# Kernel tuning notes

Measured on AMD Instinct MI355X. Metric: run time of the kernel, lower is better.

## Reference

```python
import jax, jax.numpy as jnp
import numpy as np

B, T, D = 2, 2048, 1024
H, HD = 16, 64
DL, DC = 512, 256
THETA = 10000.0
LN_EPS = 1e-5


def setup_inputs() -> dict:
    key = jax.random.key(0)
    ks = jax.random.split(key, 8)
    s = 0.02
    return {
        "x": jax.random.normal(ks[0], (B, T, D), jnp.float32),
        "W_q": jax.random.normal(ks[1], (H * HD, D), jnp.float32) * s,
        "b_q": jnp.zeros((H * HD,), jnp.float32),
        "W_kvl": jax.random.normal(ks[2], (DL, D), jnp.float32) * s,
        "b_kvl": jnp.zeros((DL,), jnp.float32),
        "ts_scale": jnp.ones((DL,), jnp.float32),
        "ts_shift": jnp.zeros((DL,), jnp.float32),
        "W_comp": jax.random.normal(ks[3], (DC, DL), jnp.float32) * s,
        "W_exp": jax.random.normal(ks[4], (DL, DC), jnp.float32) * s,
        "ln_g": jnp.ones((DC,), jnp.float32),
        "ln_b": jnp.zeros((DC,), jnp.float32),
        "W_fkv": jax.random.normal(ks[5], (2 * H * HD, DL), jnp.float32) * s,
        "b_fkv": jnp.zeros((2 * H * HD,), jnp.float32),
        "W_out": jax.random.normal(ks[6], (D, H * HD), jnp.float32) * s,
        "b_out": jnp.zeros((D,), jnp.float32),
    }


def _rope_tables(t_len):
    inv_freq = 1.0 / (THETA ** (jnp.arange(0, HD, 2, dtype=jnp.float32) / HD))
    pos = jnp.arange(t_len, dtype=jnp.float32)
    freqs = pos[:, None] * inv_freq[None, :]          # [T, HD/2]
    cos = jnp.concatenate([jnp.cos(freqs)] * 2, -1)   # [T, HD]
    sin = jnp.concatenate([jnp.sin(freqs)] * 2, -1)
    return cos[None, None], sin[None, None]           # [1,1,T,HD]


def _rotate_half(z):
    return jnp.concatenate([-z[..., HD // 2:], z[..., :HD // 2]], -1)


def reference(x, W_q, b_q, W_kvl, b_kvl, ts_scale, ts_shift, W_comp, W_exp,
              ln_g, ln_b, W_fkv, b_fkv, W_out, b_out):
    # Q path: [B,T,D] -> [B,H,T,HD]
    q = (jnp.einsum('btd,ed->bte', x, W_q) + b_q).reshape(B, T, H, HD).transpose(0, 2, 1, 3)

    # KV latent + learned KVSplice bottleneck
    kvl = jnp.einsum('btd,ld->btl', x, W_kvl) + b_kvl                 # [B,T,DL]
    xt = kvl * jax.nn.softplus(ts_scale) + ts_shift
    c = jnp.einsum('btl,cl->btc', xt, W_comp)                         # [B,T,DC]
    mu = jnp.mean(c, -1, keepdims=True)
    var = jnp.mean(jnp.square(c - mu), -1, keepdims=True)
    c = (c - mu) * jax.lax.rsqrt(var + LN_EPS) * ln_g + ln_b
    dec = jnp.einsum('btc,lc->btl', c, W_exp)                         # [B,T,DL]

    # Decompress latent to K,V
    kv = jnp.einsum('btl,el->bte', dec, W_fkv) + b_fkv                # [B,T,2*H*HD]
    kv = kv.reshape(B, T, 2, H, HD).transpose(2, 0, 3, 1, 4)          # [2,B,H,T,HD]
    k, v = kv[0], kv[1]

    # RoPE
    cos, sin = _rope_tables(T)
    q = q * cos + _rotate_half(q) * sin
    k = k * cos + _rotate_half(k) * sin

    # Causal SDPA
    scale = 1.0 / np.sqrt(HD)
    scores = jnp.einsum('bhqd,bhkd->bhqk', q, k) * scale
    mask = jnp.tril(jnp.ones((T, T), bool))
    scores = jnp.where(mask, scores, jnp.float32(-1e30))
    attn = jax.nn.softmax(scores, axis=-1)
    o = jnp.einsum('bhqk,bhkd->bhqd', attn, v)
    o = o.transpose(0, 2, 1, 3).reshape(B, T, H * HD)
    return jnp.einsum('bte,de->btd', o, W_out) + b_out
```

## Files before the change

### kernel.cpp

```cpp
#include <hip/hip_runtime.h>
#include <math.h>

#define B_SZ   2
#define T_SEQ  2048
#define NH     16
#define HDIM   64
#define D_MOD  1024
#define DL     512
#define DC     256
#define MROWS  4096

typedef __attribute__((ext_vector_type(8))) short bf16x8;
typedef __attribute__((ext_vector_type(4))) float f32x4;

#define SCALE_Q 0.18033688011112042f

static __device__ __forceinline__ unsigned short f2bf(float f) {
    union { float f; unsigned u; } v; v.f = f;
    unsigned r = v.u + 0x7fffu + ((v.u >> 16) & 1u);
    return (unsigned short)(r >> 16);
}

static __device__ __forceinline__ void gl_lds16(const unsigned short* g,
                                                unsigned short* l) {
    __builtin_amdgcn_global_load_lds(
        (const __attribute__((address_space(1))) unsigned int*)g,
        (__attribute__((address_space(3))) unsigned int*)l, 16, 0, 0);
}

__global__ __launch_bounds__(256) void cvt_bf16(
    const float* __restrict__ x,  const float* __restrict__ wq,
    const float* __restrict__ wkvl, const float* __restrict__ wcomp,
    const float* __restrict__ wexp, const float* __restrict__ wfkv,
    const float* __restrict__ wout,
    unsigned short* __restrict__ xb,  unsigned short* __restrict__ wqh,
    unsigned short* __restrict__ wkvlh, unsigned short* __restrict__ wcomph,
    unsigned short* __restrict__ wexph, unsigned short* __restrict__ wfkvh,
    unsigned short* __restrict__ wouth, float2* __restrict__ rope_tab)
{
    const int g = blockIdx.x * 256 + threadIdx.x;
    const int stride = gridDim.x * 256;
#define CVT_SEG(src, dst, n4)                                              \
    for (int i = g; i < (n4); i += stride) {                               \
        float4 v = ((const float4*)(src))[i];                              \
        unsigned short h[4] = {f2bf(v.x), f2bf(v.y), f2bf(v.z), f2bf(v.w)};\
        *(uint2*)((dst) + (size_t)i * 4) = *(uint2*)h;                     \
    }
    CVT_SEG(x, xb, 1048576)
    CVT_SEG(wq, wqh, 262144)
    CVT_SEG(wkvl, wkvlh, 131072)
    CVT_SEG(wcomp, wcomph, 32768)
    CVT_SEG(wexp, wexph, 32768)
    CVT_SEG(wfkv, wfkvh, 262144)
    CVT_SEG(wout, wouth, 262144)
#undef CVT_SEG
    for (int i = g; i < T_SEQ * 32; i += stride) {
        const int t = i >> 5, fi = i & 31;
        const float inv = __expf((float)fi * (-9.210340371976184f / 32.0f));
        float sn, cs; sincosf((float)t * inv, &sn, &cs);
        rope_tab[i] = make_float2(cs, sn);
    }
}

#define GEMM64R_PROLOG(Aptr, Wptr, Kdim)                                       \
    __shared__ unsigned short As[64 * 64];                                     \
    __shared__ unsigned short Ws[64 * 64];                                     \
    const int tid = threadIdx.x;                                               \
    const int w = tid >> 6, lane = tid & 63;                                   \
    const int l16 = lane & 15, quad = lane >> 4;                               \
    const int sw8 = ((lane & 7) ^ ((lane >> 3) & 7)) << 3;                     \
    const int srow = lane >> 3;                                                \
    const unsigned short* Ag0 = (Aptr) + (size_t)(m0 + w * 16 + srow) * (Kdim) + sw8;      \
    const unsigned short* Ag1 = (Aptr) + (size_t)(m0 + w * 16 + 8 + srow) * (Kdim) + sw8;  \
    const unsigned short* Wg0 = (Wptr) + (size_t)(n0 + w * 16 + srow) * (Kdim) + sw8;      \
    const unsigned short* Wg1 = (Wptr) + (size_t)(n0 + w * 16 + 8 + srow) * (Kdim) + sw8;  \
    unsigned short* Al0 = &As[(w * 16) * 64];                                  \
    unsigned short* Al1 = &As[(w * 16 + 8) * 64];                              \
    unsigned short* Wl0 = &Ws[(w * 16) * 64];                                  \
    unsigned short* Wl1 = &Ws[(w * 16 + 8) * 64];                              \
    const int xh = (l16 & 7);                                                  \
    f32x4 acc[4];                                                              \
    _Pragma("unroll") for (int j = 0; j < 4; ++j)                              \
        acc[j] = (f32x4){0.f, 0.f, 0.f, 0.f};                                  \
    for (int k0 = 0; k0 < (Kdim); k0 += 64) {                                  \
        __syncthreads();                                                       \
        gl_lds16(Ag0 + k0, Al0);                                               \
        gl_lds16(Ag1 + k0, Al1);                                               \
        gl_lds16(Wg0 + k0, Wl0);                                               \
        gl_lds16(Wg1 + k0, Wl1);                                               \
        __syncthreads();                                                       \
        bf16x8 af[2], bfr[4][2];                                               \
        _Pragma("unroll") for (int kk = 0; kk < 2; ++kk)                       \
            af[kk] = *(const bf16x8*)&As[(w * 16 + l16) * 64 +                 \
                                         (((kk * 4 + quad) ^ xh) << 3)];       \
        _Pragma("unroll") for (int j = 0; j < 4; ++j)                          \
            _Pragma("unroll") for (int kk = 0; kk < 2; ++kk)                   \
                bfr[j][kk] = *(const bf16x8*)&Ws[(j * 16 + l16) * 64 +         \
                                             (((kk * 4 + quad) ^ xh) << 3)];   \
        _Pragma("unroll") for (int kk = 0; kk < 2; ++kk)                       \
            _Pragma("unroll") for (int j = 0; j < 4; ++j)                      \
                acc[j] = __builtin_amdgcn_mfma_f32_16x16x32_bf16(              \
                    af[kk], bfr[j][kk], acc[j], 0, 0, 0);                      \
    }

__global__ __launch_bounds__(256) void gemm_qxt(
    const unsigned short* __restrict__ A, const unsigned short* __restrict__ Wq,
    const unsigned short* __restrict__ Wkvl,
    const float* __restrict__ b_q, const float* __restrict__ b_kvl,
    const float* __restrict__ ts_scale, const float* __restrict__ ts_shift,
    const float2* __restrict__ tab,
    unsigned short* __restrict__ qh, unsigned short* __restrict__ xt)
{
    const int m0 = blockIdx.x * 64;
    const bool is_q = (blockIdx.y < 16);
    const int n0 = is_q ? blockIdx.y * 64 : (blockIdx.y - 16) * 64;
    const unsigned short* W = is_q ? Wq : Wkvl;

    GEMM64R_PROLOG(A, W, D_MOD)

    if (is_q) {
#pragma unroll
        for (int j = 0; j < 4; ++j) {
            const int col = n0 + j * 16 + l16;
            const int h = col >> 6, hd = col & 63;
            const float bv = b_q[col];
            const float bvp = b_q[col ^ 32];
            const float sgn = (hd < 32) ? -1.f : 1.f;
#pragma unroll
            for (int reg = 0; reg < 4; ++reg) {
                const int row = m0 + w * 16 + quad * 4 + reg;
                const int b = row >> 11, t = row & (T_SEQ - 1);
                const float2 cssn = tab[t * 32 + (hd & 31)];
                const float v  = acc[j][reg] + bv;
                const float vp = acc[j ^ 2][reg] + bvp;
                const float r = (v * cssn.x + sgn * vp * cssn.y) * SCALE_Q;
                qh[(((size_t)b * NH + h) * T_SEQ + t) * HDIM + hd] = f2bf(r);
            }
        }
    } else {
#pragma unroll
        for (int j = 0; j < 4; ++j) {
            const int col = n0 + j * 16 + l16;
            const float bv = b_kvl[col];
            const float sp_s = log1pf(expf(ts_scale[col]));
            const float sp_t = ts_shift[col];
#pragma unroll
            for (int reg = 0; reg < 4; ++reg) {
                const int row = m0 + w * 16 + quad * 4 + reg;
                const float val = (acc[j][reg] + bv) * sp_s + sp_t;
                xt[(size_t)row * DL + col] = f2bf(val);
            }
        }
    }
}

__global__ __launch_bounds__(256) void gemm_kv(
    const unsigned short* __restrict__ A, const unsigned short* __restrict__ W,
    const float* __restrict__ bias, const float2* __restrict__ tab,
    unsigned short* __restrict__ kh, unsigned short* __restrict__ vth)
{
    const int m0 = blockIdx.x * 64, n0 = blockIdx.y * 64;

    GEMM64R_PROLOG(A, W, DL)

    if (n0 < 1024) {
#pragma unroll
        for (int j = 0; j < 4; ++j) {
            const int col = n0 + j * 16 + l16;
            const int h = (col >> 6) & 15, hd = col & 63;
            const float bv = bias[col];
            const float bvp = bias[col ^ 32];
            const float sgn = (hd < 32) ? -1.f : 1.f;
#pragma unroll
            for (int reg = 0; reg < 4; ++reg) {
                const int row = m0 + w * 16 + quad * 4 + reg;
                const int b = row >> 11, t = row & (T_SEQ - 1);
                const float2 cssn = tab[t * 32 + (hd & 31)];
                const float v  = acc[j][reg] + bv;
                const float vp = acc[j ^ 2][reg] + bvp;
                const float r = v * cssn.x + sgn * vp * cssn.y;
                kh[(((size_t)b * NH + h) * T_SEQ + t) * HDIM + hd] = f2bf(r);
            }
        }
    } else {
#pragma unroll
        for (int j = 0; j < 4; ++j) {
            const int col = n0 + j * 16 + l16;
            const int cv = col - 1024;
            const int h = cv >> 6, hd = cv & 63;
            const float bv = bias[col];
            unsigned short hv[4];
            const int r0 = m0 + w * 16 + quad * 4;
            const int b = r0 >> 11, t0 = r0 & (T_SEQ - 1);
#pragma unroll
            for (int reg = 0; reg < 4; ++reg)
                hv[reg] = f2bf(acc[j][reg] + bv);
            *(uint2*)&vth[(((size_t)b * NH + h) * HDIM + hd) * T_SEQ + t0] =
                *(uint2*)hv;
        }
    }
}

__global__ __launch_bounds__(256) void gemm_out(
    const unsigned short* __restrict__ A, const unsigned short* __restrict__ W,
    const float* __restrict__ bias, float* __restrict__ C)
{
    const int m0 = blockIdx.x * 64, n0 = blockIdx.y * 64;

    GEMM64R_PROLOG(A, W, D_MOD)

#pragma unroll
    for (int j = 0; j < 4; ++j) {
        const int col = n0 + j * 16 + l16;
        const float bv = bias[col];
#pragma unroll
        for (int reg = 0; reg < 4; ++reg) {
            const int row = m0 + w * 16 + quad * 4 + reg;
            C[(size_t)row * D_MOD + col] = acc[j][reg] + bv;
        }
    }
}

__global__ __launch_bounds__(256) void gemm_b(
    const unsigned short* __restrict__ A, const unsigned short* __restrict__ W,
    unsigned short* __restrict__ dec)
{
    const int m0 = blockIdx.x * 64, n0 = blockIdx.y * 64;

    GEMM64R_PROLOG(A, W, DC)

#pragma unroll
    for (int j = 0; j < 4; ++j) {
        const int col = n0 + j * 16 + l16;
#pragma unroll
        for (int reg = 0; reg < 4; ++reg) {
            const int row = m0 + w * 16 + quad * 4 + reg;
            dec[(size_t)row * DL + col] = f2bf(acc[j][reg]);
        }
    }
}

__global__ __launch_bounds__(256) void gemm_c_ln(
    const unsigned short* __restrict__ A, const unsigned short* __restrict__ W,
    const float* __restrict__ g, const float* __restrict__ bta,
    unsigned short* __restrict__ outb)
{
    __shared__ unsigned short As[16 * 32];
    __shared__ unsigned short Ws[256 * 32];
    __shared__ float redS[4][16];
    __shared__ float redQ[4][16];

    const int tid = threadIdx.x;
    const int w = tid >> 6, lane = tid & 63;
    const int l16 = lane & 15, quad = lane >> 4;
    const int m0 = blockIdx.x * 16;

    const int srow = lane >> 2, scol = (lane & 3) << 3;
    const unsigned short* Ag = A + (size_t)(m0 + srow) * DL + scol;
    const unsigned short* Wg = W + (size_t)(w * 64 + srow) * DL + scol;

    f32x4 acc[4];
#pragma unroll
    for (int j = 0; j < 4; ++j) acc[j] = (f32x4){0.f, 0.f, 0.f, 0.f};

    for (int k0 = 0; k0 < DL; k0 += 32) {
        __syncthreads();
        if (w == 0) gl_lds16(Ag + k0, &As[0]);
#pragma unroll
        for (int c = 0; c < 4; ++c)
            gl_lds16(Wg + (size_t)(c * 16) * DL + k0, &Ws[(w * 64 + c * 16) * 32]);
        __syncthreads();

        const bf16x8 af = *(const bf16x8*)&As[l16 * 32 + quad * 8];
        bf16x8 bfr[4];
#pragma unroll
        for (int j = 0; j < 4; ++j)
            bfr[j] = *(const bf16x8*)&Ws[(w * 64 + j * 16 + l16) * 32 + quad * 8];
#pragma unroll
        for (int j = 0; j < 4; ++j)
            acc[j] = __builtin_amdgcn_mfma_f32_16x16x32_bf16(af, bfr[j], acc[j], 0, 0, 0);
    }

    float s[4], q2[4];
#pragma unroll
    for (int reg = 0; reg < 4; ++reg) {
        float sv = (acc[0][reg] + acc[1][reg]) + (acc[2][reg] + acc[3][reg]);
        float qv = (acc[0][reg] * acc[0][reg] + acc[1][reg] * acc[1][reg]) +
                   (acc[2][reg] * acc[2][reg] + acc[3][reg] * acc[3][reg]);
#pragma unroll
        for (int off = 1; off < 16; off <<= 1) {
            sv += __shfl_xor(sv, off);
            qv += __shfl_xor(qv, off);
        }
        s[reg] = sv; q2[reg] = qv;
    }
    if (l16 == 0) {
#pragma unroll
        for (int reg = 0; reg < 4; ++reg) {
            redS[w][quad * 4 + reg] = s[reg];
            redQ[w][quad * 4 + reg] = q2[reg];
        }
    }
    __syncthreads();

#pragma unroll
    for (int reg = 0; reg < 4; ++reg) {
        const int r = quad * 4 + reg;
        const float sum = (redS[0][r] + redS[1][r]) + (redS[2][r] + redS[3][r]);
        const float sq  = (redQ[0][r] + redQ[1][r]) + (redQ[2][r] + redQ[3][r]);
        const float mu  = sum * (1.0f / DC);
        const float var = sq * (1.0f / DC) - mu * mu;
        const float rstd = rsqrtf(var + 1e-5f);
#pragma unroll
        for (int j = 0; j < 4; ++j) {
            const int col = w * 64 + j * 16 + l16;
            const float val = (acc[j][reg] - mu) * rstd * g[col] + bta[col];
            outb[(size_t)(m0 + r) * DC + col] = f2bf(val);
        }
    }
}

__global__ __launch_bounds__(256, 3) void flash_mfma(
    const unsigned short* __restrict__ q, const unsigned short* __restrict__ k,
    const unsigned short* __restrict__ vt, unsigned short* __restrict__ o)
{
    __shared__ unsigned short Ks[2][64 * 72];
    __shared__ unsigned short Vs[2][64 * 72];
    __shared__ unsigned short Ps[64 * 72];

    const int bh = blockIdx.x & 31;
    const int j  = 31 - (blockIdx.x >> 5);
    const int q0 = j * 64;
    const int tid = threadIdx.x;
    const int w = tid >> 6, lane = tid & 63;
    const int l16 = lane & 15, quad = lane >> 4;
    const int rbase = q0 + w * 16;

    bf16x8 qf[2];
#pragma unroll
    for (int kk = 0; kk < 2; ++kk)
        qf[kk] = *(const bf16x8*)(q + ((size_t)bh * T_SEQ + rbase + l16) * HDIM + kk * 32 + quad * 8);

    f32x4 of[4];
    float lrow[4];
#pragma unroll
    for (int dt = 0; dt < 4; ++dt) of[dt] = (f32x4){0.f, 0.f, 0.f, 0.f};
#pragma unroll
    for (int r = 0; r < 4; ++r) lrow[r] = 0.f;

    const int ldr = tid >> 2;
    const int ldc = (tid & 3) * 16;
    const unsigned short* kgb = k + ((size_t)bh * T_SEQ + ldr) * HDIM + ldc;
    const unsigned short* vgb = vt + ((size_t)bh * HDIM + ldr) * T_SEQ + ldc;

    bf16x8 kr0 = *(const bf16x8*)kgb;
    bf16x8 kr1 = *(const bf16x8*)(kgb + 8);
    bf16x8 vr0 = *(const bf16x8*)vgb;
    bf16x8 vr1 = *(const bf16x8*)(vgb + 8);

    const int kend = (j + 1) * 64;
    int buf = 0;
    for (int k0 = 0; k0 < kend; k0 += 64, buf ^= 1) {
        *(bf16x8*)&Ks[buf][ldr * 72 + ldc]     = kr0;
        *(bf16x8*)&Ks[buf][ldr * 72 + ldc + 8] = kr1;
        *(bf16x8*)&Vs[buf][ldr * 72 + ldc]     = vr0;
        *(bf16x8*)&Vs[buf][ldr * 72 + ldc + 8] = vr1;
        if (k0 + 64 < kend) {
            const unsigned short* kg = kgb + (size_t)(k0 + 64) * HDIM;
            const unsigned short* vg = vgb + (k0 + 64);
            kr0 = *(const bf16x8*)kg;
            kr1 = *(const bf16x8*)(kg + 8);
            vr0 = *(const bf16x8*)vg;
            vr1 = *(const bf16x8*)(vg + 8);
        }
        __syncthreads();

        bf16x8 kf[4][2];
#pragma unroll
        for (int nt = 0; nt < 4; ++nt)
#pragma unroll
            for (int kk = 0; kk < 2; ++kk)
                kf[nt][kk] = *(const bf16x8*)&Ks[buf][(nt * 16 + l16) * 72 + kk * 32 + quad * 8];

        f32x4 sf[4];
        __builtin_amdgcn_s_setprio(1);
#pragma unroll
        for (int nt = 0; nt < 4; ++nt) {
            sf[nt] = (f32x4){0.f, 0.f, 0.f, 0.f};
#pragma unroll
            for (int kk = 0; kk < 2; ++kk)
                sf[nt] = __builtin_amdgcn_mfma_f32_16x16x32_bf16(qf[kk], kf[nt][kk], sf[nt], 0, 0, 0);
        }
        __builtin_amdgcn_s_setprio(0);

        const bool need_mask = (k0 + 63) > rbase;
#pragma unroll
        for (int reg = 0; reg < 4; ++reg) {
            float a0 = sf[0][reg], a1 = sf[1][reg], a2 = sf[2][reg], a3 = sf[3][reg];
            if (need_mask) {
                const int tq = rbase + quad * 4 + reg;
                if (k0 +      l16 > tq) a0 = -1e30f;
                if (k0 + 16 + l16 > tq) a1 = -1e30f;
                if (k0 + 32 + l16 > tq) a2 = -1e30f;
                if (k0 + 48 + l16 > tq) a3 = -1e30f;
            }
            union { float f; unsigned u; } u0, u1, u2, u3;
            u0.f = exp2f(a0); u1.f = exp2f(a1);
            u2.f = exp2f(a2); u3.f = exp2f(a3);
            const int prow = (w * 16 + quad * 4 + reg) * 72 + l16;
            Ps[prow]      = (unsigned short)(u0.u >> 16);
            Ps[prow + 16] = (unsigned short)(u1.u >> 16);
            Ps[prow + 32] = (unsigned short)(u2.u >> 16);
            Ps[prow + 48] = (unsigned short)(u3.u >> 16);
            u0.u &= 0xffff0000u; u1.u &= 0xffff0000u;
            u2.u &= 0xffff0000u; u3.u &= 0xffff0000u;
            lrow[reg] += (u0.f + u1.f) + (u2.f + u3.f);
        }

        bf16x8 vf[4][2];
#pragma unroll
        for (int dt = 0; dt < 4; ++dt)
#pragma unroll
            for (int kk = 0; kk < 2; ++kk)
                vf[dt][kk] = *(const bf16x8*)&Vs[buf][(dt * 16 + l16) * 72 + kk * 32 + quad * 8];

        bf16x8 pf[2];
#pragma unroll
        for (int kk = 0; kk < 2; ++kk)
            pf[kk] = *(const bf16x8*)&Ps[(w * 16 + l16) * 72 + kk * 32 + quad * 8];
        __builtin_amdgcn_s_setprio(1);
#pragma unroll
        for (int dt = 0; dt < 4; ++dt)
#pragma unroll
            for (int kk = 0; kk < 2; ++kk)
                of[dt] = __builtin_amdgcn_mfma_f32_16x16x32_bf16(pf[kk], vf[dt][kk], of[dt], 0, 0, 0);
        __builtin_amdgcn_s_setprio(0);
    }

    const int b = bh >> 4, h = bh & 15;
#pragma unroll
    for (int reg = 0; reg < 4; ++reg) {
        float l = lrow[reg];
        l += __shfl_xor(l, 1);
        l += __shfl_xor(l, 2);
        l += __shfl_xor(l, 4);
        l += __shfl_xor(l, 8);
        const float inv = 1.0f / l;
        const int t = rbase + quad * 4 + reg;
#pragma unroll
        for (int dt = 0; dt < 4; ++dt)
            o[((size_t)b * T_SEQ + t) * (NH * HDIM) + h * HDIM + dt * 16 + l16] =
                f2bf(of[dt][reg] * inv);
    }
}

extern "C" void kernel_launch(void* const* d_in, const int* in_sizes, int n_in,
                              void* d_out, int out_size, void* d_ws, size_t ws_size,
                              hipStream_t stream)
{
    (void)in_sizes; (void)n_in; (void)out_size; (void)ws_size;

    const float* x        = (const float*)d_in[0];
    const float* W_q      = (const float*)d_in[1];
    const float* b_q      = (const float*)d_in[2];
    const float* W_kvl    = (const float*)d_in[3];
    const float* b_kvl    = (const float*)d_in[4];
    const float* ts_scale = (const float*)d_in[5];
    const float* ts_shift = (const float*)d_in[6];
    const float* W_comp   = (const float*)d_in[7];
    const float* W_exp    = (const float*)d_in[8];
    const float* ln_g     = (const float*)d_in[9];
    const float* ln_b     = (const float*)d_in[10];
    const float* W_fkv    = (const float*)d_in[11];
    const float* b_fkv    = (const float*)d_in[12];
    const float* W_out    = (const float*)d_in[13];
    const float* b_out    = (const float*)d_in[14];
    float* out = (float*)d_out;

    char* p = (char*)d_ws;
    unsigned short* xb     = (unsigned short*)p;             p += 8  * 1024 * 1024;
    unsigned short* wqh    = (unsigned short*)p;             p += 2  * 1024 * 1024;
    unsigned short* wkvlh  = (unsigned short*)p;             p += 1  * 1024 * 1024;
    unsigned short* wcomph = (unsigned short*)p;             p += 256 * 1024;
    unsigned short* wexph  = (unsigned short*)p;             p += 256 * 1024;
    unsigned short* wfkvh  = (unsigned short*)p;             p += 2  * 1024 * 1024;
    unsigned short* wouth  = (unsigned short*)p;             p += 2  * 1024 * 1024;
    unsigned short* qh     = (unsigned short*)p;             p += 8  * 1024 * 1024;
    unsigned short* kh     = (unsigned short*)p;             p += 8  * 1024 * 1024;
    unsigned short* vth    = (unsigned short*)p;             p += 8  * 1024 * 1024;
    unsigned short* xt     = (unsigned short*)p;             p += 4  * 1024 * 1024;
    unsigned short* cbh    = (unsigned short*)p;             p += 2  * 1024 * 1024;
    unsigned short* dec    = (unsigned short*)p;             p += 4  * 1024 * 1024;
    unsigned short* ob     = (unsigned short*)p;             p += 8  * 1024 * 1024;
    float2*         tab    = (float2*)p;                     p += 512 * 1024;

    const dim3 blk(256);

    cvt_bf16<<<1024, blk, 0, stream>>>(x, W_q, W_kvl, W_comp, W_exp, W_fkv, W_out,
                                       xb, wqh, wkvlh, wcomph, wexph, wfkvh, wouth,
                                       tab);

    gemm_qxt<<<dim3(64, 24), blk, 0, stream>>>(
        xb, wqh, wkvlh, b_q, b_kvl, ts_scale, ts_shift, tab, qh, xt);

    gemm_c_ln<<<256, blk, 0, stream>>>(
        xt, wcomph, ln_g, ln_b, cbh);

    gemm_b<<<dim3(64, 8), blk, 0, stream>>>(
        cbh, wexph, dec);

    gemm_kv<<<dim3(64, 32), blk, 0, stream>>>(
        dec, wfkvh, b_fkv, tab, kh, vth);

    flash_mfma<<<1024, blk, 0, stream>>>(qh, kh, vth, ob);

    gemm_out<<<dim3(64, 16), blk, 0, stream>>>(
        ob, wouth, b_out, out);
}
```

Before: 218.4 us.

## Enlarge flash attention query tile to 128 rows with two M-subtiles per wave

Each flash attention block now handles 128 query rows instead of 64, with each wave computing two 16-row subtiles that share the same K/V fragments loaded from LDS. This halves the K/V global loads and LDS traffic per query row and gives each wave more MFMA work per barrier. The cost is more registers per wave (lower occupancy bound of 2), a larger P buffer, half as many blocks (512), and extra wasted work on the diagonal because causal masking now happens at coarser granularity.

```diff
diff --git a/kernel.cpp b/kernel.cpp
--- a/kernel.cpp
+++ b/kernel.cpp
@@ -320,33 +320,38 @@
     }
 }
 
-__global__ __launch_bounds__(256, 3) void flash_mfma(
+__global__ __launch_bounds__(256, 2) void flash_mfma(
     const unsigned short* __restrict__ q, const unsigned short* __restrict__ k,
     const unsigned short* __restrict__ vt, unsigned short* __restrict__ o)
 {
     __shared__ unsigned short Ks[2][64 * 72];
     __shared__ unsigned short Vs[2][64 * 72];
-    __shared__ unsigned short Ps[64 * 72];
+    __shared__ unsigned short Ps[128 * 72];
 
     const int bh = blockIdx.x & 31;
-    const int j  = 31 - (blockIdx.x >> 5);
-    const int q0 = j * 64;
+    const int j  = 15 - (blockIdx.x >> 5);
+    const int q0 = j * 128;
     const int tid = threadIdx.x;
     const int w = tid >> 6, lane = tid & 63;
     const int l16 = lane & 15, quad = lane >> 4;
-    const int rbase = q0 + w * 16;
-
-    bf16x8 qf[2];
-#pragma unroll
-    for (int kk = 0; kk < 2; ++kk)
-        qf[kk] = *(const bf16x8*)(q + ((size_t)bh * T_SEQ + rbase + l16) * HDIM + kk * 32 + quad * 8);
-
-    f32x4 of[4];
-    float lrow[4];
-#pragma unroll
-    for (int dt = 0; dt < 4; ++dt) of[dt] = (f32x4){0.f, 0.f, 0.f, 0.f};
-#pragma unroll
-    for (int r = 0; r < 4; ++r) lrow[r] = 0.f;
+    const int rbase = q0 + w * 32;
+
+    bf16x8 qf[2][2];
+#pragma unroll
+    for (int mi = 0; mi < 2; ++mi)
+#pragma unroll
+        for (int kk = 0; kk < 2; ++kk)
+            qf[mi][kk] = *(const bf16x8*)(q + ((size_t)bh * T_SEQ + rbase + mi * 16 + l16) * HDIM + kk * 32 + quad * 8);
+
+    f32x4 of[2][4];
+    float lrow[2][4];
+#pragma unroll
+    for (int mi = 0; mi < 2; ++mi) {
+#pragma unroll
+        for (int dt = 0; dt < 4; ++dt) of[mi][dt] = (f32x4){0.f, 0.f, 0.f, 0.f};
+#pragma unroll
+        for (int r = 0; r < 4; ++r) lrow[mi][r] = 0.f;
+    }
 
     const int ldr = tid >> 2;
     const int ldc = (tid & 3) * 16;
@@ -358,7 +363,7 @@
     bf16x8 vr0 = *(const bf16x8*)vgb;
     bf16x8 vr1 = *(const bf16x8*)(vgb + 8);
 
-    const int kend = (j + 1) * 64;
+    const int kend = q0 + 128;
     int buf = 0;
     for (int k0 = 0; k0 < kend; k0 += 64, buf ^= 1) {
         *(bf16x8*)&Ks[buf][ldr * 72 + ldc]     = kr0;
@@ -382,39 +387,46 @@
             for (int kk = 0; kk < 2; ++kk)
                 kf[nt][kk] = *(const bf16x8*)&Ks[buf][(nt * 16 + l16) * 72 + kk * 32 + quad * 8];
 
-        f32x4 sf[4];
+        f32x4 sf[2][4];
         __builtin_amdgcn_s_setprio(1);
 #pragma unroll
-        for (int nt = 0; nt < 4; ++nt) {
-            sf[nt] = (f32x4){0.f, 0.f, 0.f, 0.f};
-#pragma unroll
-            for (int kk = 0; kk < 2; ++kk)
-                sf[nt] = __builtin_amdgcn_mfma_f32_16x16x32_bf16(qf[kk], kf[nt][kk], sf[nt], 0, 0, 0);
-        }
+        for (int mi = 0; mi < 2; ++mi)
+#pragma unroll
+            for (int nt = 0; nt < 4; ++nt) {
+                sf[mi][nt] = (f32x4){0.f, 0.f, 0.f, 0.f};
+#pragma unroll
+                for (int kk = 0; kk < 2; ++kk)
+                    sf[mi][nt] = __builtin_amdgcn_mfma_f32_16x16x32_bf16(qf[mi][kk], kf[nt][kk], sf[mi][nt], 0, 0, 0);
+            }
         __builtin_amdgcn_s_setprio(0);
 
-        const bool need_mask = (k0 + 63) > rbase;
-#pragma unroll
-        for (int reg = 0; reg < 4; ++reg) {
-            float a0 = sf[0][reg], a1 = sf[1][reg], a2 = sf[2][reg], a3 = sf[3][reg];
-            if (need_mask) {
-                const int tq = rbase + quad * 4 + reg;
-                if (k0 +      l16 > tq) a0 = -1e30f;
-                if (k0 + 16 + l16 > tq) a1 = -1e30f;
-                if (k0 + 32 + l16 > tq) a2 = -1e30f;
-                if (k0 + 48 + l16 > tq) a3 = -1e30f;
+#pragma unroll
+        for (int mi = 0; mi < 2; ++mi) {
+            const int mb = rbase + mi * 16;
+            const bool need_mask = (k0 + 63) > mb;
+#pragma unroll
+            for (int reg = 0; reg < 4; ++reg) {
+                float a0 = sf[mi][0][reg], a1 = sf[mi][1][reg];
+                float a2 = sf[mi][2][reg], a3 = sf[mi][3][reg];
+                if (need_mask) {
+                    const int tq = mb + quad * 4 + reg;
+                    if (k0 +      l16 > tq) a0 = -1e30f;
+                    if (k0 + 16 + l16 > tq) a1 = -1e30f;
+                    if (k0 + 32 + l16 > tq) a2 = -1e30f;
+                    if (k0 + 48 + l16 > tq) a3 = -1e30f;
+                }
+                union { float f; unsigned u; } u0, u1, u2, u3;
+                u0.f = exp2f(a0); u1.f = exp2f(a1);
+                u2.f = exp2f(a2); u3.f = exp2f(a3);
+                const int prow = (w * 32 + mi * 16 + quad * 4 + reg) * 72 + l16;
+                Ps[prow]      = (unsigned short)(u0.u >> 16);
+                Ps[prow + 16] = (unsigned short)(u1.u >> 16);
+                Ps[prow + 32] = (unsigned short)(u2.u >> 16);
+                Ps[prow + 48] = (unsigned short)(u3.u >> 16);
+                u0.u &= 0xffff0000u; u1.u &= 0xffff0000u;
+                u2.u &= 0xffff0000u; u3.u &= 0xffff0000u;
+                lrow[mi][reg] += (u0.f + u1.f) + (u2.f + u3.f);
             }
-            union { float f; unsigned u; } u0, u1, u2, u3;
-            u0.f = exp2f(a0); u1.f = exp2f(a1);
-            u2.f = exp2f(a2); u3.f = exp2f(a3);
-            const int prow = (w * 16 + quad * 4 + reg) * 72 + l16;
-            Ps[prow]      = (unsigned short)(u0.u >> 16);
-            Ps[prow + 16] = (unsigned short)(u1.u >> 16);
-            Ps[prow + 32] = (unsigned short)(u2.u >> 16);
-            Ps[prow + 48] = (unsigned short)(u3.u >> 16);
-            u0.u &= 0xffff0000u; u1.u &= 0xffff0000u;
-            u2.u &= 0xffff0000u; u3.u &= 0xffff0000u;
-            lrow[reg] += (u0.f + u1.f) + (u2.f + u3.f);
         }
 
         bf16x8 vf[4][2];
@@ -424,33 +436,39 @@
             for (int kk = 0; kk < 2; ++kk)
                 vf[dt][kk] = *(const bf16x8*)&Vs[buf][(dt * 16 + l16) * 72 + kk * 32 + quad * 8];
 
-        bf16x8 pf[2];
-#pragma unroll
-        for (int kk = 0; kk < 2; ++kk)
-            pf[kk] = *(const bf16x8*)&Ps[(w * 16 + l16) * 72 + kk * 32 + quad * 8];
+        bf16x8 pf[2][2];
+#pragma unroll
+        for (int mi = 0; mi < 2; ++mi)
+#pragma unroll
+            for (int kk = 0; kk < 2; ++kk)
+                pf[mi][kk] = *(const bf16x8*)&Ps[(w * 32 + mi * 16 + l16) * 72 + kk * 32 + quad * 8];
         __builtin_amdgcn_s_setprio(1);
 #pragma unroll
-        for (int dt = 0; dt < 4; ++dt)
-#pragma unroll
-            for (int kk = 0; kk < 2; ++kk)
-                of[dt] = __builtin_amdgcn_mfma_f32_16x16x32_bf16(pf[kk], vf[dt][kk], of[dt], 0, 0, 0);
+        for (int mi = 0; mi < 2; ++mi)
+#pragma unroll
+            for (int dt = 0; dt < 4; ++dt)
+#pragma unroll
+                for (int kk = 0; kk < 2; ++kk)
+                    of[mi][dt] = __builtin_amdgcn_mfma_f32_16x16x32_bf16(pf[mi][kk], vf[dt][kk], of[mi][dt], 0, 0, 0);
         __builtin_amdgcn_s_setprio(0);
     }
 
     const int b = bh >> 4, h = bh & 15;
 #pragma unroll
+    for (int mi = 0; mi < 2; ++mi)
+#pragma unroll
     for (int reg = 0; reg < 4; ++reg) {
-        float l = lrow[reg];
+        float l = lrow[mi][reg];
         l += __shfl_xor(l, 1);
         l += __shfl_xor(l, 2);
         l += __shfl_xor(l, 4);
         l += __shfl_xor(l, 8);
         const float inv = 1.0f / l;
-        const int t = rbase + quad * 4 + reg;
+        const int t = rbase + mi * 16 + quad * 4 + reg;
 #pragma unroll
         for (int dt = 0; dt < 4; ++dt)
             o[((size_t)b * T_SEQ + t) * (NH * HDIM) + h * HDIM + dt * 16 + l16] =
-                f2bf(of[dt][reg] * inv);
+                f2bf(of[mi][dt][reg] * inv);
     }
 }
 
@@ -512,7 +530,7 @@
     gemm_kv<<<dim3(64, 32), blk, 0, stream>>>(
         dec, wfkvh, b_fkv, tab, kh, vth);
 
-    flash_mfma<<<1024, blk, 0, stream>>>(qh, kh, vth, ob);
+    flash_mfma<<<512, blk, 0, stream>>>(qh, kh, vth, ob);
 
     gemm_out<<<dim3(64, 16), blk, 0, stream>>>(
         ob, wouth, b_out, out);
```

Measured after the change: 232.0 us. 6.2% more time.

## Double-buffer LDS tiles in shared GEMM prolog to overlap loads with MFMA

Applied to the files above, without the earlier changes.

Replaces the single-buffered GEMM main loop used by four GEMM kernels with a two-stage LDS ping-pong. The next K-tile's direct global-to-LDS loads are issued before computing the current tile, with explicit vmcnt waits and raw s_barrier replacing __syncthreads. This aims to hide global load latency behind MFMA work, at the cost of doubling LDS per block (32 KB), which may reduce occupancy.

```diff
diff --git a/kernel.cpp b/kernel.cpp
--- a/kernel.cpp
+++ b/kernel.cpp
@@ -62,45 +62,52 @@
     }
 }
 
-#define GEMM64R_PROLOG(Aptr, Wptr, Kdim)                                       \
-    __shared__ unsigned short As[64 * 64];                                     \
-    __shared__ unsigned short Ws[64 * 64];                                     \
+#define GEMM64P_PROLOG(Aptr, Wptr, Kdim)                                       \
+    __shared__ unsigned short As[2][64 * 64];                                  \
+    __shared__ unsigned short Ws[2][64 * 64];                                  \
     const int tid = threadIdx.x;                                               \
     const int w = tid >> 6, lane = tid & 63;                                   \
     const int l16 = lane & 15, quad = lane >> 4;                               \
     const int sw8 = ((lane & 7) ^ ((lane >> 3) & 7)) << 3;                     \
     const int srow = lane >> 3;                                                \
     const unsigned short* Ag0 = (Aptr) + (size_t)(m0 + w * 16 + srow) * (Kdim) + sw8;      \
-    const unsigned short* Ag1 = (Aptr) + (size_t)(m0 + w * 16 + 8 + srow) * (Kdim) + sw8;  \
+    const unsigned short* Ag1 = Ag0 + (size_t)8 * (Kdim);                      \
     const unsigned short* Wg0 = (Wptr) + (size_t)(n0 + w * 16 + srow) * (Kdim) + sw8;      \
-    const unsigned short* Wg1 = (Wptr) + (size_t)(n0 + w * 16 + 8 + srow) * (Kdim) + sw8;  \
-    unsigned short* Al0 = &As[(w * 16) * 64];                                  \
-    unsigned short* Al1 = &As[(w * 16 + 8) * 64];                              \
-    unsigned short* Wl0 = &Ws[(w * 16) * 64];                                  \
-    unsigned short* Wl1 = &Ws[(w * 16 + 8) * 64];                              \
+    const unsigned short* Wg1 = Wg0 + (size_t)8 * (Kdim);                      \
+    const int aoff = (w * 16) * 64;                                            \
     const int xh = (l16 & 7);                                                  \
     f32x4 acc[4];                                                              \
     _Pragma("unroll") for (int j = 0; j < 4; ++j)                              \
         acc[j] = (f32x4){0.f, 0.f, 0.f, 0.f};                                  \
-    for (int k0 = 0; k0 < (Kdim); k0 += 64) {                                  \
-        __syncthreads();                                                       \
-        gl_lds16(Ag0 + k0, Al0);                                               \
-        gl_lds16(Ag1 + k0, Al1);                                               \
-        gl_lds16(Wg0 + k0, Wl0);                                               \
-        gl_lds16(Wg1 + k0, Wl1);                                               \
-        __syncthreads();                                                       \
+    gl_lds16(Ag0, &As[0][aoff]);                                               \
+    gl_lds16(Ag1, &As[0][aoff + 512]);                                         \
+    gl_lds16(Wg0, &Ws[0][aoff]);                                               \
+    gl_lds16(Wg1, &Ws[0][aoff + 512]);                                         \
+    for (int k0 = 0, buf = 0; k0 < (Kdim); k0 += 64, buf ^= 1) {               \
+        if (k0 + 64 < (Kdim)) {                                                \
+            gl_lds16(Ag0 + k0 + 64, &As[buf ^ 1][aoff]);                       \
+            gl_lds16(Ag1 + k0 + 64, &As[buf ^ 1][aoff + 512]);                 \
+            gl_lds16(Wg0 + k0 + 64, &Ws[buf ^ 1][aoff]);                       \
+            gl_lds16(Wg1 + k0 + 64, &Ws[buf ^ 1][aoff + 512]);                 \
+            asm volatile("s_waitcnt vmcnt(4)" ::: "memory");                   \
+        } else {                                                               \
+            asm volatile("s_waitcnt vmcnt(0)" ::: "memory");                   \
+        }                                                                      \
+        __builtin_amdgcn_s_barrier();                                          \
         bf16x8 af[2], bfr[4][2];                                               \
         _Pragma("unroll") for (int kk = 0; kk < 2; ++kk)                       \
-            af[kk] = *(const bf16x8*)&As[(w * 16 + l16) * 64 +                 \
+            af[kk] = *(const bf16x8*)&As[buf][(w * 16 + l16) * 64 +            \
                                          (((kk * 4 + quad) ^ xh) << 3)];       \
         _Pragma("unroll") for (int j = 0; j < 4; ++j)                          \
             _Pragma("unroll") for (int kk = 0; kk < 2; ++kk)                   \
-                bfr[j][kk] = *(const bf16x8*)&Ws[(j * 16 + l16) * 64 +         \
+                bfr[j][kk] = *(const bf16x8*)&Ws[buf][(j * 16 + l16) * 64 +    \
                                              (((kk * 4 + quad) ^ xh) << 3)];   \
         _Pragma("unroll") for (int kk = 0; kk < 2; ++kk)                       \
             _Pragma("unroll") for (int j = 0; j < 4; ++j)                      \
                 acc[j] = __builtin_amdgcn_mfma_f32_16x16x32_bf16(              \
                     af[kk], bfr[j][kk], acc[j], 0, 0, 0);                      \
+        asm volatile("s_waitcnt lgkmcnt(0)" ::: "memory");                     \
+        __builtin_amdgcn_s_barrier();                                          \
     }
 
 __global__ __launch_bounds__(256) void gemm_qxt(
@@ -116,7 +123,7 @@
     const int n0 = is_q ? blockIdx.y * 64 : (blockIdx.y - 16) * 64;
     const unsigned short* W = is_q ? Wq : Wkvl;
 
-    GEMM64R_PROLOG(A, W, D_MOD)
+    GEMM64P_PROLOG(A, W, D_MOD)
 
     if (is_q) {
 #pragma unroll
@@ -161,7 +168,7 @@
 {
     const int m0 = blockIdx.x * 64, n0 = blockIdx.y * 64;
 
-    GEMM64R_PROLOG(A, W, DL)
+    GEMM64P_PROLOG(A, W, DL)
 
     if (n0 < 1024) {
 #pragma unroll
@@ -207,7 +214,7 @@
 {
     const int m0 = blockIdx.x * 64, n0 = blockIdx.y * 64;
 
-    GEMM64R_PROLOG(A, W, D_MOD)
+    GEMM64P_PROLOG(A, W, D_MOD)
 
 #pragma unroll
     for (int j = 0; j < 4; ++j) {
@@ -227,7 +234,7 @@
 {
     const int m0 = blockIdx.x * 64, n0 = blockIdx.y * 64;
 
-    GEMM64R_PROLOG(A, W, DC)
+    GEMM64P_PROLOG(A, W, DC)
 
 #pragma unroll
     for (int j = 0; j < 4; ++j) {
```

New measurement: 219.5 us. About the same (+0.5%).
